# Performance work log

Measured on AMD Instinct MI355X. Metric: run time of the kernel, lower is better.

## Reference

```python
import jax, jax.numpy as jnp
import numpy as np

N_NODES = 100000
N_EDGES = 3200000
EMBED = 64
DIMS = [(64, 32), (32, 16)]  # (in_dim, out_dim) per Aggregator layer
EPS = 1e-12


def setup_inputs() -> dict:
    key = jax.random.key(0)
    ks = jax.random.split(key, 16)
    inp = {
        "aux_info_all": jax.random.normal(ks[0], (N_NODES, 3), jnp.float32),
        "entity_embed": jax.random.normal(ks[1], (N_NODES, EMBED), jnp.float32) * 0.1,
        "aux_W": jax.random.normal(ks[2], (EMBED, 3), jnp.float32) * 0.3,
        "aux_b": jnp.zeros((EMBED,), jnp.float32),
        "edge_vals": jax.random.uniform(ks[3], (N_EDGES,), jnp.float32),
        "edge_rows": jax.random.randint(ks[4], (N_EDGES,), 0, N_NODES, jnp.int32),
        "edge_cols": jax.random.randint(ks[5], (N_EDGES,), 0, N_NODES, jnp.int32),
    }
    for li, (din, dout) in enumerate(DIMS):
        s = (2.0 / (din + dout)) ** 0.5  # xavier-ish scale
        inp[f"W1_{li}"] = jax.random.normal(ks[6 + 4 * li], (dout, din), jnp.float32) * s
        inp[f"b1_{li}"] = jnp.zeros((dout,), jnp.float32)
        inp[f"W2_{li}"] = jax.random.normal(ks[7 + 4 * li], (dout, din), jnp.float32) * s
        inp[f"b2_{li}"] = jnp.zeros((dout,), jnp.float32)
    return inp


def _l2norm(x):
    return x / jnp.maximum(jnp.linalg.norm(x, axis=1, keepdims=True), EPS)


def reference(aux_info_all, entity_embed, aux_W, aux_b,
              W1_0, b1_0, W2_0, b2_0, W1_1, b1_1, W2_1, b2_1,
              edge_vals, edge_rows, edge_cols):
    # holographic fusion: entity_embed * (1 + tanh(Linear(aux)))
    aux_vec = jnp.tanh(aux_info_all @ aux_W.T + aux_b)
    ego = entity_embed * (1.0 + aux_vec)  # [N, 64]
    all_embed = [ego]
    layers = [(W1_0, b1_0, W2_0, b2_0), (W1_1, b1_1, W2_1, b2_1)]
    for W1, b1, W2, b2 in layers:
        # sparse A_in @ ego: gather messages over edges, segment-sum by destination row
        msgs = edge_vals[:, None] * ego[edge_cols]  # [E, d]
        side = jax.ops.segment_sum(msgs, edge_rows, num_segments=N_NODES)  # [N, d]
        sum_e = jax.nn.leaky_relu((ego + side) @ W1.T + b1)  # bi-interaction branch 1
        bi_e = jax.nn.leaky_relu((ego * side) @ W2.T + b2)   # bi-interaction branch 2
        ego = sum_e + bi_e  # (dropout p=0 in eval)
        all_embed.append(_l2norm(ego))
    return jnp.concatenate(all_embed, axis=1)  # [N, 64+32+16]
```

## Files before the change

kernel.cpp:

```cpp
#include <hip/hip_runtime.h>
#include <math.h>

#define NN 100000
#define NE 3200000
#define OUTD 112
#define BROWS 512
#define NBUCK 196
#define FILL_CH 8192
#define FILL_B ((NE + FILL_CH - 1) / FILL_CH)
#define BLD1_T 1024
#define SORT_T 512

__device__ inline unsigned short f32_to_bf16(float f) {
    unsigned u = __float_as_uint(f);
    u += 0x7FFFu + ((u >> 16) & 1u);
    return (unsigned short)(u >> 16);
}
__device__ inline float bf16_bits_to_f32(unsigned b) {
    return __uint_as_float(b << 16);
}

__global__ void fuse_ego_kernel(const float* __restrict__ aux_info,
                                const float* __restrict__ entity,
                                const float* __restrict__ aux_W,
                                const float* __restrict__ aux_b,
                                unsigned short* __restrict__ ego0h,
                                float* __restrict__ out) {
    int idx = blockIdx.x * blockDim.x + threadIdx.x;
    if (idx >= NN * 64) return;
    int n = idx >> 6;
    int j = idx & 63;
    float a0 = aux_info[n * 3 + 0];
    float a1 = aux_info[n * 3 + 1];
    float a2 = aux_info[n * 3 + 2];
    float w0 = aux_W[j * 3 + 0];
    float w1 = aux_W[j * 3 + 1];
    float w2 = aux_W[j * 3 + 2];
    float t = tanhf(fmaf(a0, w0, fmaf(a1, w1, fmaf(a2, w2, aux_b[j]))));
    float e = entity[idx] * (1.0f + t);
    ego0h[idx] = f32_to_bf16(e);
    out[(size_t)n * OUTD + j] = e;
}

__global__ void bhist_kernel(const int* __restrict__ rows, int* __restrict__ gcount) {
    __shared__ int h[NBUCK];
    for (int i = threadIdx.x; i < NBUCK; i += BLD1_T) h[i] = 0;
    __syncthreads();
    int base = blockIdx.x * FILL_CH;
    int nE = NE - base; if (nE > FILL_CH) nE = FILL_CH;
    for (int i = threadIdx.x; i < nE; i += BLD1_T)
        atomicAdd(&h[rows[base + i] >> 9], 1);
    __syncthreads();
    for (int i = threadIdx.x; i < NBUCK; i += BLD1_T)
        if (h[i]) atomicAdd(&gcount[i], h[i]);
}

__global__ void bscan_kernel(const int* __restrict__ gcount,
                             int* __restrict__ bucket_base,
                             int* __restrict__ gcursor) {
    __shared__ int sh[256];
    int t = threadIdx.x;
    int v = (t < NBUCK) ? gcount[t] : 0;
    sh[t] = v;
    __syncthreads();
    for (int off = 1; off < 256; off <<= 1) {
        int u = (t >= off) ? sh[t - off] : 0;
        __syncthreads();
        sh[t] += u;
        __syncthreads();
    }
    if (t < NBUCK) {
        int excl = sh[t] - v;
        bucket_base[t] = excl;
        gcursor[t] = excl;
    }
    if (t == 255) bucket_base[NBUCK] = sh[255];
}

__global__ void bucket_fill_kernel(const int* __restrict__ rows,
                                   const int* __restrict__ cols,
                                   const float* __restrict__ vals,
                                   int* __restrict__ gcursor,
                                   int2* __restrict__ edges_b) {
    __shared__ int rowsL[FILL_CH];
    __shared__ int hcnt[NBUCK];
    __shared__ int curs[NBUCK];
    int base = blockIdx.x * FILL_CH;
    int nE = NE - base; if (nE > FILL_CH) nE = FILL_CH;
    for (int i = threadIdx.x; i < NBUCK; i += BLD1_T) hcnt[i] = 0;
    __syncthreads();
    for (int i = threadIdx.x; i < nE; i += BLD1_T) {
        int r = rows[base + i];
        rowsL[i] = r;
        atomicAdd(&hcnt[r >> 9], 1);
    }
    __syncthreads();
    for (int b = threadIdx.x; b < NBUCK; b += BLD1_T) {
        int c = hcnt[b];
        curs[b] = c ? atomicAdd(&gcursor[b], c) : 0;
    }
    __syncthreads();
    for (int i = threadIdx.x; i < nE; i += BLD1_T) {
        int r = rowsL[i];
        int b = r >> 9;
        int p = atomicAdd(&curs[b], 1);
        edges_b[p] = make_int2(cols[base + i] | ((r & (BROWS - 1)) << 17),
                               __float_as_int(vals[base + i]));
    }
}

__global__ void csr_sort_kernel(const int2* __restrict__ edges_b,
                                const int* __restrict__ bucket_base,
                                unsigned int* __restrict__ edges,
                                int* __restrict__ row_ptr) {
    __shared__ int cnt[BROWS];
    __shared__ int scn[BROWS];
    __shared__ int curs[BROWS];
    int b = blockIdx.x;
    int beg = bucket_base[b], end = bucket_base[b + 1];
    int t = threadIdx.x;
    cnt[t] = 0;
    __syncthreads();
    for (int i = beg + t; i < end; i += SORT_T)
        atomicAdd(&cnt[(edges_b[i].x >> 17) & (BROWS - 1)], 1);
    __syncthreads();
    scn[t] = cnt[t];
    __syncthreads();
    for (int off = 1; off < BROWS; off <<= 1) {
        int v = (t >= off) ? scn[t - off] : 0;
        __syncthreads();
        scn[t] += v;
        __syncthreads();
    }
    {
        int excl = scn[t] - cnt[t];
        int n = b * BROWS + t;
        if (n <= NN) row_ptr[n] = beg + excl;
        curs[t] = beg + excl;
    }
    __syncthreads();
    for (int i = beg + t; i < end; i += SORT_T) {
        int2 e = edges_b[i];
        int rl = (e.x >> 17) & (BROWS - 1);
        int p = atomicAdd(&curs[rl], 1);
        unsigned int vb = f32_to_bf16(__int_as_float(e.y)) & 0x7FFFu;
        edges[p] = (unsigned int)(e.x & 0x1FFFF) | (vb << 17);
    }
}

template <int D>
__global__ __launch_bounds__(256) void gather_kernel(
    const uint4* __restrict__ egoh4,
    const unsigned int* __restrict__ edges,
    const int* __restrict__ row_ptr,
    float* __restrict__ side) {
    constexpr int FO = D / 8;
    constexpr int ES = 32 / FO;
    constexpr int U  = 16 / ES;
    const int gt = blockIdx.x * 256 + threadIdx.x;
    const int n  = gt >> 5;
    const int li = gt & 31;
    const int es = li / FO;
    const int fo = li % FO;
    if (n >= NN) return;
    int beg = row_ptr[n];
    int end = row_ptr[n + 1];
    float a[8] = {0.f, 0.f, 0.f, 0.f, 0.f, 0.f, 0.f, 0.f};
    int i = beg;
    for (; i + U * ES <= end; i += U * ES) {
        unsigned ew[U];
        uint4 g[U];
#pragma unroll
        for (int u = 0; u < U; ++u) ew[u] = edges[i + u * ES + es];
#pragma unroll
        for (int u = 0; u < U; ++u)
            g[u] = egoh4[(size_t)(ew[u] & 0x1FFFFu) * FO + fo];
#pragma unroll
        for (int u = 0; u < U; ++u) {
            float v = __uint_as_float((ew[u] >> 1) & 0xFFFF0000u);
            a[0] = fmaf(v, __uint_as_float(g[u].x << 16), a[0]);
            a[1] = fmaf(v, __uint_as_float(g[u].x & 0xFFFF0000u), a[1]);
            a[2] = fmaf(v, __uint_as_float(g[u].y << 16), a[2]);
            a[3] = fmaf(v, __uint_as_float(g[u].y & 0xFFFF0000u), a[3]);
            a[4] = fmaf(v, __uint_as_float(g[u].z << 16), a[4]);
            a[5] = fmaf(v, __uint_as_float(g[u].z & 0xFFFF0000u), a[5]);
            a[6] = fmaf(v, __uint_as_float(g[u].w << 16), a[6]);
            a[7] = fmaf(v, __uint_as_float(g[u].w & 0xFFFF0000u), a[7]);
        }
    }
    for (; i + ES <= end; i += ES) {
        unsigned ew = edges[i + es];
        uint4 g = egoh4[(size_t)(ew & 0x1FFFFu) * FO + fo];
        float v = __uint_as_float((ew >> 1) & 0xFFFF0000u);
        a[0] = fmaf(v, __uint_as_float(g.x << 16), a[0]);
        a[1] = fmaf(v, __uint_as_float(g.x & 0xFFFF0000u), a[1]);
        a[2] = fmaf(v, __uint_as_float(g.y << 16), a[2]);
        a[3] = fmaf(v, __uint_as_float(g.y & 0xFFFF0000u), a[3]);
        a[4] = fmaf(v, __uint_as_float(g.z << 16), a[4]);
        a[5] = fmaf(v, __uint_as_float(g.z & 0xFFFF0000u), a[5]);
        a[6] = fmaf(v, __uint_as_float(g.w << 16), a[6]);
        a[7] = fmaf(v, __uint_as_float(g.w & 0xFFFF0000u), a[7]);
    }
    if (i + es < end) {
        unsigned ew = edges[i + es];
        uint4 g = egoh4[(size_t)(ew & 0x1FFFFu) * FO + fo];
        float v = __uint_as_float((ew >> 1) & 0xFFFF0000u);
        a[0] = fmaf(v, __uint_as_float(g.x << 16), a[0]);
        a[1] = fmaf(v, __uint_as_float(g.x & 0xFFFF0000u), a[1]);
        a[2] = fmaf(v, __uint_as_float(g.y << 16), a[2]);
        a[3] = fmaf(v, __uint_as_float(g.y & 0xFFFF0000u), a[3]);
        a[4] = fmaf(v, __uint_as_float(g.z << 16), a[4]);
        a[5] = fmaf(v, __uint_as_float(g.z & 0xFFFF0000u), a[5]);
        a[6] = fmaf(v, __uint_as_float(g.w << 16), a[6]);
        a[7] = fmaf(v, __uint_as_float(g.w & 0xFFFF0000u), a[7]);
    }
#pragma unroll
    for (int st = FO; st < 32; st <<= 1) {
#pragma unroll
        for (int q = 0; q < 8; ++q) a[q] += __shfl_xor(a[q], st);
    }
    if (es == 0)
        *(float4*)&side[(size_t)n * D + fo * 8] =
            make_float4(a[0], a[1], a[2], a[3]);
    else if (es == 1)
        *(float4*)&side[(size_t)n * D + fo * 8 + 4] =
            make_float4(a[4], a[5], a[6], a[7]);
}

template <int DIN, int DOUT, int NB>
__global__ __launch_bounds__(256, 4) void layer_kernel(
    const float* __restrict__ ego, int ego_stride,
    const float* __restrict__ side,
    const float* __restrict__ W1, const float* __restrict__ b1,
    const float* __restrict__ W2, const float* __restrict__ b2,
    float* __restrict__ ego_next,
    unsigned short* __restrict__ ego_next_h,
    float* __restrict__ out, int out_off)
{
    constexpr int RW  = DIN + 4;
    constexpr int CH  = DIN / 4;
    constexpr int NPT = NB * DOUT / 256;
    static_assert(NB * DOUT % 256 == 0, "");
    static_assert(NPT == 4, "register budget tuned for NPT=4");

    __shared__ float sArr[NB][RW];
    __shared__ float pArr[NB][RW];
    __shared__ float4 W1q[CH * DOUT];
    __shared__ float4 W2q[CH * DOUT];

    const int node0 = blockIdx.x * NB;

    for (int t = threadIdx.x; t < CH * DOUT; t += 256) {
        int j  = t / CH;
        int kg = t - j * CH;
        W1q[kg * DOUT + j] = *(const float4*)&W1[j * DIN + kg * 4];
        W2q[kg * DOUT + j] = *(const float4*)&W2[j * DIN + kg * 4];
    }

    for (int i = threadIdx.x; i < NB * CH; i += 256) {
        int m = i / CH;
        int c = i - m * CH;
        int n = node0 + m;
        if (n < NN) {
            float4 e  = *(const float4*)&ego[(size_t)n * ego_stride + c * 4];
            float4 sd = *(const float4*)&side[(size_t)n * DIN + c * 4];
            *(float4*)&sArr[m][c * 4] =
                make_float4(e.x + sd.x, e.y + sd.y, e.z + sd.z, e.w + sd.w);
            *(float4*)&pArr[m][c * 4] =
                make_float4(e.x * sd.x, e.y * sd.y, e.z * sd.z, e.w * sd.w);
        }
    }
    __syncthreads();

    const int j     = threadIdx.x % DOUT;
    const int slot  = threadIdx.x / DOUT;
    const int mbase = slot * NPT;

    float acc1[NPT], acc2[NPT];
    {
        float bb1 = b1[j], bb2 = b2[j];
#pragma unroll
        for (int m8 = 0; m8 < NPT; ++m8) { acc1[m8] = bb1; acc2[m8] = bb2; }
    }

#pragma unroll 2
    for (int kg = 0; kg < CH; ++kg) {
        float4 w1 = W1q[kg * DOUT + j];
        float4 w2 = W2q[kg * DOUT + j];
#pragma unroll
        for (int m8 = 0; m8 < NPT; ++m8) {
            float4 sv = *(const float4*)&sArr[mbase + m8][kg * 4];
            float4 pv = *(const float4*)&pArr[mbase + m8][kg * 4];
            acc1[m8] = fmaf(sv.x, w1.x, acc1[m8]);
            acc1[m8] = fmaf(sv.y, w1.y, acc1[m8]);
            acc1[m8] = fmaf(sv.z, w1.z, acc1[m8]);
            acc1[m8] = fmaf(sv.w, w1.w, acc1[m8]);
            acc2[m8] = fmaf(pv.x, w2.x, acc2[m8]);
            acc2[m8] = fmaf(pv.y, w2.y, acc2[m8]);
            acc2[m8] = fmaf(pv.z, w2.z, acc2[m8]);
            acc2[m8] = fmaf(pv.w, w2.w, acc2[m8]);
        }
    }

#pragma unroll
    for (int m8 = 0; m8 < NPT; ++m8) {
        int n = node0 + mbase + m8;
        float s  = acc1[m8]; s  = (s  > 0.0f) ? s  : 0.01f * s;
        float bb = acc2[m8]; bb = (bb > 0.0f) ? bb : 0.01f * bb;
        float v = s + bb;
        float sq = v * v;
#pragma unroll
        for (int off = DOUT / 2; off > 0; off >>= 1)
            sq += __shfl_xor(sq, off, DOUT);
        float norm = sqrtf(sq);
        norm = (norm > 1e-12f) ? norm : 1e-12f;
        if (n < NN) {
            if (ego_next)   ego_next[(size_t)n * DOUT + j] = v;
            if (ego_next_h) ego_next_h[(size_t)n * DOUT + j] = f32_to_bf16(v);
            out[(size_t)n * OUTD + out_off + j] = v / norm;
        }
    }
}

extern "C" void kernel_launch(void* const* d_in, const int* in_sizes, int n_in,
                              void* d_out, int out_size, void* d_ws, size_t ws_size,
                              hipStream_t stream) {
    const float* aux_info  = (const float*)d_in[0];
    const float* entity    = (const float*)d_in[1];
    const float* aux_W     = (const float*)d_in[2];
    const float* aux_b     = (const float*)d_in[3];
    const float* edge_vals = (const float*)d_in[4];
    const int*   edge_rows = (const int*)d_in[5];
    const int*   edge_cols = (const int*)d_in[6];
    const float* W1_0 = (const float*)d_in[7];
    const float* b1_0 = (const float*)d_in[8];
    const float* W2_0 = (const float*)d_in[9];
    const float* b2_0 = (const float*)d_in[10];
    const float* W1_1 = (const float*)d_in[11];
    const float* b1_1 = (const float*)d_in[12];
    const float* W2_1 = (const float*)d_in[13];
    const float* b2_1 = (const float*)d_in[14];
    float* out = (float*)d_out;

    float* region0 = (float*)d_ws;
    int2*  edges_b = (int2*)region0;
    float* side0   = region0;
    unsigned short* ego0h = (unsigned short*)(region0 + (size_t)NE * 2);
    unsigned short* ego1h = ego0h;
    unsigned int* edges = (unsigned int*)((float*)ego0h + (size_t)NN * 32);
    float* ego1  = (float*)(edges + NE);
    float* side1 = ego1 + (size_t)NN * 32;
    int* row_ptr     = (int*)(side1 + (size_t)NN * 32);
    int* bucket_base = row_ptr + NN + 1;
    int* gcount      = bucket_base + NBUCK + 1;

    hipMemsetAsync(gcount, 0, (size_t)NBUCK * sizeof(int), stream);
    bhist_kernel<<<FILL_B, BLD1_T, 0, stream>>>(edge_rows, gcount);
    bscan_kernel<<<1, 256, 0, stream>>>(gcount, bucket_base, gcount);
    bucket_fill_kernel<<<FILL_B, BLD1_T, 0, stream>>>(
        edge_rows, edge_cols, edge_vals, gcount, edges_b);
    csr_sort_kernel<<<NBUCK, SORT_T, 0, stream>>>(edges_b, bucket_base, edges, row_ptr);

    {
        int total = NN * 64;
        fuse_ego_kernel<<<(total + 255) / 256, 256, 0, stream>>>(
            aux_info, entity, aux_W, aux_b, ego0h, out);
    }
    gather_kernel<64><<<NN / 8, 256, 0, stream>>>(
        (const uint4*)ego0h, edges, row_ptr, side0);
    layer_kernel<64, 32, 32><<<(NN + 31) / 32, 256, 0, stream>>>(
        out, OUTD, side0, W1_0, b1_0, W2_0, b2_0, ego1, ego1h, out, 64);
    gather_kernel<32><<<NN / 8, 256, 0, stream>>>(
        (const uint4*)ego1h, edges, row_ptr, side1);
    layer_kernel<32, 16, 64><<<(NN + 63) / 64, 256, 0, stream>>>(
        ego1, 32, side1, W1_1, b1_1, W2_1, b2_1, nullptr, nullptr, out, 96);
}
```

Measured before the change: 385.1 us.

## Precompute per-block bucket cursors via transposed histogram scan; deepen gather unrolling

The histogram kernel now writes each block's per-bucket counts to a transposed table. A new scan kernel turns that table into deterministic per-block, per-bucket write cursors, so the fill kernel no longer recomputes its local histogram, keeps no row staging buffer in shared memory, and issues no global atomics. The gather kernel's main loop now takes 32 edges per step, falling back to 16 and then to one per lane, to put more loads in flight. This adds one small kernel launch, and the larger unroll raises register use.

```diff
diff --git a/kernel.cpp b/kernel.cpp
--- a/kernel.cpp
+++ b/kernel.cpp
@@ -42,7 +42,9 @@
     out[(size_t)n * OUTD + j] = e;
 }
 
-__global__ void bhist_kernel(const int* __restrict__ rows, int* __restrict__ gcount) {
+__global__ void bhist_kernel(const int* __restrict__ rows,
+                             int* __restrict__ gcount,
+                             int* __restrict__ bhistT) {
     __shared__ int h[NBUCK];
     for (int i = threadIdx.x; i < NBUCK; i += BLD1_T) h[i] = 0;
     __syncthreads();
@@ -51,13 +53,15 @@
     for (int i = threadIdx.x; i < nE; i += BLD1_T)
         atomicAdd(&h[rows[base + i] >> 9], 1);
     __syncthreads();
-    for (int i = threadIdx.x; i < NBUCK; i += BLD1_T)
-        if (h[i]) atomicAdd(&gcount[i], h[i]);
+    for (int i = threadIdx.x; i < NBUCK; i += BLD1_T) {
+        int c = h[i];
+        bhistT[i * FILL_B + blockIdx.x] = c;
+        if (c) atomicAdd(&gcount[i], c);
+    }
 }
 
 __global__ void bscan_kernel(const int* __restrict__ gcount,
-                             int* __restrict__ bucket_base,
-                             int* __restrict__ gcursor) {
+                             int* __restrict__ bucket_base) {
     __shared__ int sh[256];
     int t = threadIdx.x;
     int v = (t < NBUCK) ? gcount[t] : 0;
@@ -69,41 +73,43 @@
         sh[t] += u;
         __syncthreads();
     }
-    if (t < NBUCK) {
-        int excl = sh[t] - v;
-        bucket_base[t] = excl;
-        gcursor[t] = excl;
-    }
+    if (t < NBUCK) bucket_base[t] = sh[t] - v;
     if (t == 255) bucket_base[NBUCK] = sh[255];
+}
+
+__global__ void cursor_scan_kernel(const int* __restrict__ bhistT,
+                                   const int* __restrict__ bucket_base,
+                                   int* __restrict__ cursor) {
+    static_assert(FILL_B <= 512, "scan width");
+    __shared__ int sh[512];
+    int b = blockIdx.x;
+    int t = threadIdx.x;
+    int v = (t < FILL_B) ? bhistT[b * FILL_B + t] : 0;
+    sh[t] = v;
+    __syncthreads();
+    for (int off = 1; off < 512; off <<= 1) {
+        int u = (t >= off) ? sh[t - off] : 0;
+        __syncthreads();
+        sh[t] += u;
+        __syncthreads();
+    }
+    if (t < FILL_B) cursor[b * FILL_B + t] = bucket_base[b] + sh[t] - v;
 }
 
 __global__ void bucket_fill_kernel(const int* __restrict__ rows,
                                    const int* __restrict__ cols,
                                    const float* __restrict__ vals,
-                                   int* __restrict__ gcursor,
+                                   const int* __restrict__ cursor,
                                    int2* __restrict__ edges_b) {
-    __shared__ int rowsL[FILL_CH];
-    __shared__ int hcnt[NBUCK];
     __shared__ int curs[NBUCK];
     int base = blockIdx.x * FILL_CH;
     int nE = NE - base; if (nE > FILL_CH) nE = FILL_CH;
-    for (int i = threadIdx.x; i < NBUCK; i += BLD1_T) hcnt[i] = 0;
+    for (int i = threadIdx.x; i < NBUCK; i += BLD1_T)
+        curs[i] = cursor[i * FILL_B + blockIdx.x];
     __syncthreads();
     for (int i = threadIdx.x; i < nE; i += BLD1_T) {
         int r = rows[base + i];
-        rowsL[i] = r;
-        atomicAdd(&hcnt[r >> 9], 1);
-    }
-    __syncthreads();
-    for (int b = threadIdx.x; b < NBUCK; b += BLD1_T) {
-        int c = hcnt[b];
-        curs[b] = c ? atomicAdd(&gcursor[b], c) : 0;
-    }
-    __syncthreads();
-    for (int i = threadIdx.x; i < nE; i += BLD1_T) {
-        int r = rowsL[i];
-        int b = r >> 9;
-        int p = atomicAdd(&curs[b], 1);
+        int p = atomicAdd(&curs[r >> 9], 1);
         edges_b[p] = make_int2(cols[base + i] | ((r & (BROWS - 1)) << 17),
                                __float_as_int(vals[base + i]));
     }
@@ -148,6 +154,32 @@
     }
 }
 
+template <int FO, int UU>
+__device__ __forceinline__ void gacc(const uint4* __restrict__ egoh4,
+                                     const unsigned int* __restrict__ edges,
+                                     int i, int es, int fo, float a[8]) {
+    constexpr int ES = 32 / FO;
+    unsigned ew[UU];
+    uint4 g[UU];
+#pragma unroll
+    for (int u = 0; u < UU; ++u) ew[u] = edges[i + u * ES + es];
+#pragma unroll
+    for (int u = 0; u < UU; ++u)
+        g[u] = egoh4[(size_t)(ew[u] & 0x1FFFFu) * FO + fo];
+#pragma unroll
+    for (int u = 0; u < UU; ++u) {
+        float v = __uint_as_float((ew[u] >> 1) & 0xFFFF0000u);
+        a[0] = fmaf(v, __uint_as_float(g[u].x << 16), a[0]);
+        a[1] = fmaf(v, __uint_as_float(g[u].x & 0xFFFF0000u), a[1]);
+        a[2] = fmaf(v, __uint_as_float(g[u].y << 16), a[2]);
+        a[3] = fmaf(v, __uint_as_float(g[u].y & 0xFFFF0000u), a[3]);
+        a[4] = fmaf(v, __uint_as_float(g[u].z << 16), a[4]);
+        a[5] = fmaf(v, __uint_as_float(g[u].z & 0xFFFF0000u), a[5]);
+        a[6] = fmaf(v, __uint_as_float(g[u].w << 16), a[6]);
+        a[7] = fmaf(v, __uint_as_float(g[u].w & 0xFFFF0000u), a[7]);
+    }
+}
+
 template <int D>
 __global__ __launch_bounds__(256) void gather_kernel(
     const uint4* __restrict__ egoh4,
@@ -156,7 +188,6 @@
     float* __restrict__ side) {
     constexpr int FO = D / 8;
     constexpr int ES = 32 / FO;
-    constexpr int U  = 16 / ES;
     const int gt = blockIdx.x * 256 + threadIdx.x;
     const int n  = gt >> 5;
     const int li = gt & 31;
@@ -167,40 +198,9 @@
     int end = row_ptr[n + 1];
     float a[8] = {0.f, 0.f, 0.f, 0.f, 0.f, 0.f, 0.f, 0.f};
     int i = beg;
-    for (; i + U * ES <= end; i += U * ES) {
-        unsigned ew[U];
-        uint4 g[U];
-#pragma unroll
-        for (int u = 0; u < U; ++u) ew[u] = edges[i + u * ES + es];
-#pragma unroll
-        for (int u = 0; u < U; ++u)
-            g[u] = egoh4[(size_t)(ew[u] & 0x1FFFFu) * FO + fo];
-#pragma unroll
-        for (int u = 0; u < U; ++u) {
-            float v = __uint_as_float((ew[u] >> 1) & 0xFFFF0000u);
-            a[0] = fmaf(v, __uint_as_float(g[u].x << 16), a[0]);
-            a[1] = fmaf(v, __uint_as_float(g[u].x & 0xFFFF0000u), a[1]);
-            a[2] = fmaf(v, __uint_as_float(g[u].y << 16), a[2]);
-            a[3] = fmaf(v, __uint_as_float(g[u].y & 0xFFFF0000u), a[3]);
-            a[4] = fmaf(v, __uint_as_float(g[u].z << 16), a[4]);
-            a[5] = fmaf(v, __uint_as_float(g[u].z & 0xFFFF0000u), a[5]);
-            a[6] = fmaf(v, __uint_as_float(g[u].w << 16), a[6]);
-            a[7] = fmaf(v, __uint_as_float(g[u].w & 0xFFFF0000u), a[7]);
-        }
-    }
-    for (; i + ES <= end; i += ES) {
-        unsigned ew = edges[i + es];
-        uint4 g = egoh4[(size_t)(ew & 0x1FFFFu) * FO + fo];
-        float v = __uint_as_float((ew >> 1) & 0xFFFF0000u);
-        a[0] = fmaf(v, __uint_as_float(g.x << 16), a[0]);
-        a[1] = fmaf(v, __uint_as_float(g.x & 0xFFFF0000u), a[1]);
-        a[2] = fmaf(v, __uint_as_float(g.y << 16), a[2]);
-        a[3] = fmaf(v, __uint_as_float(g.y & 0xFFFF0000u), a[3]);
-        a[4] = fmaf(v, __uint_as_float(g.z << 16), a[4]);
-        a[5] = fmaf(v, __uint_as_float(g.z & 0xFFFF0000u), a[5]);
-        a[6] = fmaf(v, __uint_as_float(g.w << 16), a[6]);
-        a[7] = fmaf(v, __uint_as_float(g.w & 0xFFFF0000u), a[7]);
-    }
+    for (; i + 32 <= end; i += 32) gacc<FO, 32 / ES>(egoh4, edges, i, es, fo, a);
+    for (; i + 16 <= end; i += 16) gacc<FO, 16 / ES>(egoh4, edges, i, es, fo, a);
+    for (; i + ES <= end; i += ES) gacc<FO, 1>(egoh4, edges, i, es, fo, a);
     if (i + es < end) {
         unsigned ew = edges[i + es];
         uint4 g = egoh4[(size_t)(ew & 0x1FFFFu) * FO + fo];
@@ -353,12 +353,15 @@
     int* row_ptr     = (int*)(side1 + (size_t)NN * 32);
     int* bucket_base = row_ptr + NN + 1;
     int* gcount      = bucket_base + NBUCK + 1;
+    int* bhistT      = gcount + NBUCK;
+    int* cursor      = bhistT + (size_t)NBUCK * FILL_B;
 
     hipMemsetAsync(gcount, 0, (size_t)NBUCK * sizeof(int), stream);
-    bhist_kernel<<<FILL_B, BLD1_T, 0, stream>>>(edge_rows, gcount);
-    bscan_kernel<<<1, 256, 0, stream>>>(gcount, bucket_base, gcount);
+    bhist_kernel<<<FILL_B, BLD1_T, 0, stream>>>(edge_rows, gcount, bhistT);
+    bscan_kernel<<<1, 256, 0, stream>>>(gcount, bucket_base);
+    cursor_scan_kernel<<<NBUCK, 512, 0, stream>>>(bhistT, bucket_base, cursor);
     bucket_fill_kernel<<<FILL_B, BLD1_T, 0, stream>>>(
-        edge_rows, edge_cols, edge_vals, gcount, edges_b);
+        edge_rows, edge_cols, edge_vals, cursor, edges_b);
     csr_sort_kernel<<<NBUCK, SORT_T, 0, stream>>>(edges_b, bucket_base, edges, row_ptr);
 
     {
```

Result: slower. 394.6 us (+2.5%).
